# Kernel tuning notes

Hardware: AMD Instinct MI355X
Metric: run time of the kernel (lower is better)

## Reference

```python
import jax, jax.numpy as jnp
import numpy as np
from jax import lax

BIG = 1e6  # sentinel 1D distance when no zero seen yet (squared stays finite in fp32)


def edt_2d(binary):
    """Exact Euclidean distance transform of a (B, H, W) binary image.

    Matches scipy.ndimage.distance_transform_edt: for each nonzero pixel,
    distance to the nearest zero pixel. Separable formulation:
      pass 1: g[b,i,c]   = min_r |i - r| s.t. binary[b,r,c] == 0   (two scans)
      pass 2: d2[b,i,j]  = min_c g[b,i,c]^2 + (j - c)^2            (broadcast-min)
    """
    B, H, W = binary.shape
    xs = jnp.moveaxis(binary, 1, 0)  # (H, B, W) -> scan over rows

    def sweep(carry, x):
        d = jnp.where(x == 0, 0.0, carry + 1.0)
        return d, d

    init = jnp.full((B, W), BIG, dtype=binary.dtype)
    _, down = lax.scan(sweep, init, xs)
    _, up = lax.scan(sweep, init, xs, reverse=True)
    g = jnp.moveaxis(jnp.minimum(down, up), 0, 1)  # (B, H, W) vertical 1D EDT

    j = jnp.arange(W, dtype=binary.dtype)
    diff2 = (j[:, None] - j[None, :]) ** 2  # (W_out, W_src)
    # (B, H, 1, W) + (W, W) -> min over source column axis
    d2 = jnp.min(g[:, :, None, :] ** 2 + diff2[None, None, :, :], axis=-1)
    return jnp.sqrt(d2)


def combo_loss(pred, target,
               dice_weight=0.5, bce_weight=0.5, boundary_weight=0.1, focal_weight=0.2,
               smooth=1.0, alpha=1.0, gamma=2.0, inner_boundary_weight=1.0):
    p = jax.nn.sigmoid(pred)

    # Dice
    intersection = jnp.sum(p * target)
    union = jnp.sum(p) + jnp.sum(target)
    dice = 1.0 - (2.0 * intersection + smooth) / (union + smooth)

    # BCEWithLogits (stable)
    bce = jnp.mean(jnp.maximum(pred, 0.0) - pred * target
                   + jnp.log1p(jnp.exp(-jnp.abs(pred))))

    # Boundary loss (torch thresholds raw pred > 0.5, detached -> stop_gradient)
    pred_bin = lax.stop_gradient((pred > 0.5).astype(pred.dtype))[:, 0]    # (B,H,W)
    targ_bin = lax.stop_gradient(target.astype(pred.dtype))[:, 0]          # (B,H,W)
    # per-sample mean then batch mean == global mean (equal-size images)
    boundary = inner_boundary_weight * jnp.mean(
        jnp.abs(edt_2d(pred_bin) - edt_2d(targ_bin)))

    # Focal
    bce_el = -(target * jnp.log(p) + (1.0 - target) * jnp.log(1.0 - p))
    pt = p * target + (1.0 - p) * (1.0 - target)
    focal = jnp.mean(alpha * (1.0 - pt) ** gamma * bce_el)

    return (dice_weight * dice + bce_weight * bce
            + boundary_weight * boundary + focal_weight * focal)


def setup_inputs() -> dict:
    key = jax.random.key(0)
    k1, k2 = jax.random.split(key)
    B, C, H, W = 4, 1, 256, 256
    pred = jax.random.normal(k1, (B, C, H, W), dtype=jnp.float32)
    target = jax.random.bernoulli(k2, 0.5, (B, C, H, W)).astype(jnp.float32)
    return {"pred": pred, "target": target}


def reference(pred, target):
    return combo_loss(pred, target)
```

## Files before the change

kernel.cpp:

```cpp
#include <hip/hip_runtime.h>
#include <math.h>

#define BB 4
#define HH 256
#define WW 256
#define NN (BB*HH*WW)
typedef unsigned long long u64;
typedef unsigned int u32;

#define SENT 100000


__global__ __launch_bounds__(512)
void fused_main(const float* __restrict__ pred,
                const float* __restrict__ targ,
                float* __restrict__ partial) {
    __shared__ float G[2][4][WW];
    __shared__ float D[2][4][WW];
    __shared__ float red[8][6];

    int blk  = blockIdx.x;
    int b    = blk >> 6;
    int band = blk & 63;
    int i0   = band << 2;
    int wq   = i0 >> 6;
    int o0   = i0 & 63;

    int tid  = threadIdx.x;
    int img  = tid >> 8;
    int c    = tid & 255;

    const float* s = (img ? targ : pred) + b * (HH * WW) + c;
    u64 M[4];
    #pragma unroll
    for (int w = 0; w < 4; ++w) {
        u64 m = 0;
        #pragma unroll
        for (int rr = 0; rr < 64; ++rr) {
            float x = s[(w * 64 + rr) * WW];
            m |= ((u64)(x <= 0.5f)) << rr;
        }
        M[w] = m;
    }

    {
        u64 M0 = M[0], M1 = M[1], M2 = M[2], M3 = M[3];

        int t1 = __ffsll(M1), t2 = __ffsll(M2), t3 = __ffsll(M3);
        int f1 = t1 ? 64 + t1 - 1  : SENT;
        int f2 = t2 ? 128 + t2 - 1 : SENT;
        int f3 = t3 ? 192 + t3 - 1 : SENT;
        int r0 = __ffsll(__brevll(M0));
        int r1 = __ffsll(__brevll(M1));
        int r2 = __ffsll(__brevll(M2));
        int l0 = r0 ? 64 - r0  : -SENT;
        int l1 = r1 ? 128 - r1 : -SENT;
        int l2 = r2 ? 192 - r2 : -SENT;

        int s3 = f3;
        int s2 = min(f2, s3);
        int s1 = min(f1, s2);
        int NF = (wq == 0) ? s1 : (wq == 1) ? s2 : (wq == 2) ? s3 : SENT;
        int q0 = l0;
        int q1 = max(q0, l1);
        int q2 = max(q1, l2);
        int PB = (wq == 0) ? -SENT : (wq == 1) ? q0 : (wq == 2) ? q1 : q2;
        u64 Mq = (wq == 0) ? M0 : (wq == 1) ? M1 : (wq == 2) ? M2 : M3;

        #pragma unroll
        for (int kk = 0; kk < 4; ++kk) {
            int i = i0 + kk, o = o0 + kk;
            u64 sh  = Mq >> o;
            int tn  = __ffsll(sh);
            int n   = tn ? i + tn - 1 : NF;
            u64 shl = Mq << (63 - o);
            int tp  = __ffsll(__brevll(shl));
            int p   = tp ? i - (tp - 1) : PB;
            int g   = min(n - i, i - p);
            G[img][kk][c] = (float)g * (float)g;
        }
    }
    __syncthreads();

    {
        int j = c;
        float d2[4];
        #pragma unroll
        for (int k = 0; k < 4; ++k)
            d2[k] = G[img][k][j];
        for (int r = 1; r < WW; ++r) {
            float r2 = (float)(r * r);
            float dmax = fmaxf(fmaxf(d2[0], d2[1]), fmaxf(d2[2], d2[3]));
            if (__all(r2 >= dmax)) break;
            int lo = j - r, hi = j + r;
            if (lo >= 0) {
                #pragma unroll
                for (int k = 0; k < 4; ++k)
                    d2[k] = fminf(d2[k], G[img][k][lo] + r2);
            }
            if (hi < WW) {
                #pragma unroll
                for (int k = 0; k < 4; ++k)
                    d2[k] = fminf(d2[k], G[img][k][hi] + r2);
            }
        }
        #pragma unroll
        for (int k = 0; k < 4; ++k)
            D[img][k][j] = sqrtf(d2[k]);
    }
    __syncthreads();

    float sPT = 0.0f, sP = 0.0f, sT = 0.0f, sBCE = 0.0f, sFOC = 0.0f, sBND = 0.0f;
    #pragma unroll
    for (int h = 0; h < 2; ++h) {
        int q  = tid + h * 512;
        int k  = q >> 8;
        int j2 = q & 255;
        int idx = (b * HH + (i0 + k)) * WW + j2;
        float x = pred[idx];
        float t = targ[idx];

        sBND += fabsf(D[0][k][j2] - D[1][k][j2]);

        float p   = 1.0f / (1.0f + expf(-x));
        float ax  = fabsf(x);
        float l1p = log1pf(expf(-ax));
        float bce_el = fmaxf(x, 0.0f) - x * t + l1p;
        float lsx  = fminf(x, 0.0f) - l1p;
        float lsnx = -fmaxf(x, 0.0f) - l1p;
        float bce_f = -(t * lsx + (1.0f - t) * lsnx);
        float pt = p * t + (1.0f - p) * (1.0f - t);
        float om = 1.0f - pt;

        sPT  += p * t;
        sP   += p;
        sT   += t;
        sBCE += bce_el;
        sFOC += om * om * bce_f;
    }

    float vals[6] = { sPT, sP, sT, sBCE, sFOC, sBND };
    int lane = tid & 63;
    int wave = tid >> 6;
    #pragma unroll
    for (int k = 0; k < 6; ++k) {
        float v = vals[k];
        #pragma unroll
        for (int off = 32; off > 0; off >>= 1)
            v += __shfl_down(v, off, 64);
        if (lane == 0) red[wave][k] = v;
    }
    __syncthreads();
    if (tid < 6) {
        float s2 = 0.0f;
        #pragma unroll
        for (int wv = 0; wv < 8; ++wv) s2 += red[wv][tid];
        partial[blk * 8 + tid] = s2;
    }
}

__global__ __launch_bounds__(256)
void finalize(const float* __restrict__ partial, float* __restrict__ out) {
    __shared__ float red[4][6];
    int tid = threadIdx.x;
    float v[6];
    #pragma unroll
    for (int k = 0; k < 6; ++k) v[k] = partial[tid * 8 + k];

    int lane = tid & 63;
    int wave = tid >> 6;
    #pragma unroll
    for (int k = 0; k < 6; ++k) {
        float x = v[k];
        #pragma unroll
        for (int off = 32; off > 0; off >>= 1)
            x += __shfl_down(x, off, 64);
        if (lane == 0) red[wave][k] = x;
    }
    __syncthreads();
    if (tid == 0) {
        float inter = red[0][0] + red[1][0] + red[2][0] + red[3][0];
        float sp    = red[0][1] + red[1][1] + red[2][1] + red[3][1];
        float st    = red[0][2] + red[1][2] + red[2][2] + red[3][2];
        float bce   = red[0][3] + red[1][3] + red[2][3] + red[3][3];
        float foc   = red[0][4] + red[1][4] + red[2][4] + red[3][4];
        float bnd   = red[0][5] + red[1][5] + red[2][5] + red[3][5];
        float invN = 1.0f / (float)NN;
        float dice = 1.0f - (2.0f * inter + 1.0f) / (sp + st + 1.0f);
        out[0] = 0.5f * dice + 0.5f * (bce * invN)
               + 0.1f * (bnd * invN) + 0.2f * (foc * invN);
    }
}

extern "C" void kernel_launch(void* const* d_in, const int* in_sizes, int n_in,
                              void* d_out, int out_size, void* d_ws, size_t ws_size,
                              hipStream_t stream) {
    (void)in_sizes; (void)n_in; (void)out_size; (void)ws_size;
    const float* pred = (const float*)d_in[0];
    const float* targ = (const float*)d_in[1];
    float* ws = (float*)d_ws;

    fused_main<<<256, 512, 0, stream>>>(pred, targ, ws);
    finalize<<<1, 256, 0, stream>>>(ws, (float*)d_out);
}
```

Baseline: 68.48 us.

## Vectorize column mask loads via shared transpose and fuse finalize with ticket

Each thread now builds the per-column zero bitmasks from float4 row loads covering four columns and one quarter of the rows. The masks are transposed through shared memory (padded stride) so each column thread can still read its four 64-bit words. The elementwise pass uses float2 loads issued early. The separate finalize kernel is replaced by a last-block-done pattern with a global ticket counter and threadfence, which removes one launch but adds an atomic, an extra barrier and a larger shared-memory footprint.

```diff
diff --git a/kernel.cpp b/kernel.cpp
--- a/kernel.cpp
+++ b/kernel.cpp
@@ -10,14 +10,19 @@
 
 #define SENT 100000
 
+__device__ unsigned g_ticket = 0u;
+
 
 __global__ __launch_bounds__(512)
-void fused_main(const float* __restrict__ pred,
-                const float* __restrict__ targ,
-                float* __restrict__ partial) {
+void fused_all(const float* __restrict__ pred,
+               const float* __restrict__ targ,
+               float* __restrict__ partial,
+               float* __restrict__ out) {
+    __shared__ u32   MSK[2][WW][9];
     __shared__ float G[2][4][WW];
     __shared__ float D[2][4][WW];
     __shared__ float red[8][6];
+    __shared__ int   amLast;
 
     int blk  = blockIdx.x;
     int b    = blk >> 6;
@@ -28,23 +33,44 @@
 
     int tid  = threadIdx.x;
     int img  = tid >> 8;
-    int c    = tid & 255;
-
-    const float* s = (img ? targ : pred) + b * (HH * WW) + c;
-    u64 M[4];
-    #pragma unroll
-    for (int w = 0; w < 4; ++w) {
-        u64 m = 0;
+
+    int k4   = tid >> 7;
+    int j4   = (tid << 1) & 255;
+    int idx4 = (b * HH + (i0 + k4)) * WW + j4;
+    float2 xv = *(const float2*)(pred + idx4);
+    float2 tv = *(const float2*)(targ + idx4);
+
+    {
+        int r8 = tid & 255;
+        int w  = r8 >> 6;
+        int c4 = r8 & 63;
+        const float* s = (img ? targ : pred) + b * (HH * WW)
+                       + (w * 64) * WW + (c4 * 4);
+        u64 m0 = 0, m1 = 0, m2 = 0, m3 = 0;
         #pragma unroll
         for (int rr = 0; rr < 64; ++rr) {
-            float x = s[(w * 64 + rr) * WW];
-            m |= ((u64)(x <= 0.5f)) << rr;
-        }
-        M[w] = m;
-    }
-
+            float4 v = *(const float4*)(s + rr * WW);
+            m0 |= ((u64)(v.x <= 0.5f)) << rr;
+            m1 |= ((u64)(v.y <= 0.5f)) << rr;
+            m2 |= ((u64)(v.z <= 0.5f)) << rr;
+            m3 |= ((u64)(v.w <= 0.5f)) << rr;
+        }
+        u64 mm[4] = { m0, m1, m2, m3 };
+        #pragma unroll
+        for (int k = 0; k < 4; ++k) {
+            MSK[img][c4 * 4 + k][2 * w]     = (u32)mm[k];
+            MSK[img][c4 * 4 + k][2 * w + 1] = (u32)(mm[k] >> 32);
+        }
+    }
+    __syncthreads();
+
+    int c = tid & 255;
     {
-        u64 M0 = M[0], M1 = M[1], M2 = M[2], M3 = M[3];
+        const u32* mp = MSK[img][c];
+        u64 M0 = (u64)mp[0] | ((u64)mp[1] << 32);
+        u64 M1 = (u64)mp[2] | ((u64)mp[3] << 32);
+        u64 M2 = (u64)mp[4] | ((u64)mp[5] << 32);
+        u64 M3 = (u64)mp[6] | ((u64)mp[7] << 32);
 
         int t1 = __ffsll(M1), t2 = __ffsll(M2), t3 = __ffsll(M3);
         int f1 = t1 ? 64 + t1 - 1  : SENT;
@@ -112,15 +138,11 @@
 
     float sPT = 0.0f, sP = 0.0f, sT = 0.0f, sBCE = 0.0f, sFOC = 0.0f, sBND = 0.0f;
     #pragma unroll
-    for (int h = 0; h < 2; ++h) {
-        int q  = tid + h * 512;
-        int k  = q >> 8;
-        int j2 = q & 255;
-        int idx = (b * HH + (i0 + k)) * WW + j2;
-        float x = pred[idx];
-        float t = targ[idx];
-
-        sBND += fabsf(D[0][k][j2] - D[1][k][j2]);
+    for (int e = 0; e < 2; ++e) {
+        float x = e ? xv.y : xv.x;
+        float t = e ? tv.y : tv.x;
+
+        sBND += fabsf(D[0][k4][j4 + e] - D[1][k4][j4 + e]);
 
         float p   = 1.0f / (1.0f + expf(-x));
         float ax  = fabsf(x);
@@ -151,44 +173,51 @@
         if (lane == 0) red[wave][k] = v;
     }
     __syncthreads();
-    if (tid < 6) {
-        float s2 = 0.0f;
-        #pragma unroll
-        for (int wv = 0; wv < 8; ++wv) s2 += red[wv][tid];
-        partial[blk * 8 + tid] = s2;
-    }
-}
-
-__global__ __launch_bounds__(256)
-void finalize(const float* __restrict__ partial, float* __restrict__ out) {
-    __shared__ float red[4][6];
-    int tid = threadIdx.x;
-    float v[6];
-    #pragma unroll
-    for (int k = 0; k < 6; ++k) v[k] = partial[tid * 8 + k];
-
-    int lane = tid & 63;
-    int wave = tid >> 6;
-    #pragma unroll
-    for (int k = 0; k < 6; ++k) {
-        float x = v[k];
-        #pragma unroll
-        for (int off = 32; off > 0; off >>= 1)
-            x += __shfl_down(x, off, 64);
-        if (lane == 0) red[wave][k] = x;
-    }
-    __syncthreads();
+
     if (tid == 0) {
-        float inter = red[0][0] + red[1][0] + red[2][0] + red[3][0];
-        float sp    = red[0][1] + red[1][1] + red[2][1] + red[3][1];
-        float st    = red[0][2] + red[1][2] + red[2][2] + red[3][2];
-        float bce   = red[0][3] + red[1][3] + red[2][3] + red[3][3];
-        float foc   = red[0][4] + red[1][4] + red[2][4] + red[3][4];
-        float bnd   = red[0][5] + red[1][5] + red[2][5] + red[3][5];
-        float invN = 1.0f / (float)NN;
-        float dice = 1.0f - (2.0f * inter + 1.0f) / (sp + st + 1.0f);
-        out[0] = 0.5f * dice + 0.5f * (bce * invN)
-               + 0.1f * (bnd * invN) + 0.2f * (foc * invN);
+        #pragma unroll
+        for (int k = 0; k < 6; ++k) {
+            float s = 0.0f;
+            #pragma unroll
+            for (int wv = 0; wv < 8; ++wv) s += red[wv][k];
+            partial[blk * 8 + k] = s;
+        }
+        __threadfence();
+        unsigned old = atomicAdd(&g_ticket, 1u);
+        amLast = ((old & 255u) == 255u) ? 1 : 0;
+    }
+    __syncthreads();
+
+    if (amLast) {
+        float v[6] = { 0, 0, 0, 0, 0, 0 };
+        if (tid < 256) {
+            float* ps = partial + tid * 8;
+            #pragma unroll
+            for (int k = 0; k < 6; ++k)
+                v[k] = atomicAdd(&ps[k], 0.0f);
+        }
+        #pragma unroll
+        for (int k = 0; k < 6; ++k) {
+            float x = v[k];
+            #pragma unroll
+            for (int off = 32; off > 0; off >>= 1)
+                x += __shfl_down(x, off, 64);
+            if (lane == 0) red[wave][k] = x;
+        }
+        __syncthreads();
+        if (tid == 0) {
+            float s[6];
+            #pragma unroll
+            for (int k = 0; k < 6; ++k)
+                s[k] = red[0][k] + red[1][k] + red[2][k] + red[3][k]
+                     + red[4][k] + red[5][k] + red[6][k] + red[7][k];
+            float inter = s[0], sp = s[1], st = s[2];
+            float bce = s[3], foc = s[4], bnd = s[5];
+            float invN = 1.0f / (float)NN;
+            float dice = 1.0f - (2.0f * inter + 1.0f) / (sp + st + 1.0f);
+            out[0] = 0.5f * dice + 0.5f * (bce * invN)
+                   + 0.1f * (bnd * invN) + 0.2f * (foc * invN);
+        }
     }
 }
 
@@ -200,6 +229,5 @@
     const float* targ = (const float*)d_in[1];
     float* ws = (float*)d_ws;
 
-    fused_main<<<256, 512, 0, stream>>>(pred, targ, ws);
-    finalize<<<1, 256, 0, stream>>>(ws, (float*)d_out);
+    fused_all<<<256, 512, 0, stream>>>(pred, targ, ws, (float*)d_out);
 }
```

Result: slower. 73.13 us (+6.8%).
